# Kernel tuning notes

Measured on AMD Instinct MI355X. Metric: run time of the kernel, lower is better.

## Reference

```python
import jax, jax.numpy as jnp
import numpy as np

N_NODES = 50000
N_EDGES = 1600000
IN_DIM = 128
N_HEADS = 8
OUT_DIM = 16


def setup_inputs() -> dict:
    key = jax.random.key(0)
    ks = jax.random.split(key, 9)
    scale = 1.0 / np.sqrt(IN_DIM)
    return {
        "state": jax.random.normal(ks[0], (N_NODES, IN_DIM), dtype=jnp.float32),
        "src": jax.random.randint(ks[1], (N_EDGES,), 0, N_NODES, dtype=jnp.int32),
        "dst": jax.random.randint(ks[2], (N_EDGES,), 0, N_NODES, dtype=jnp.int32),
        "WQ": jax.random.normal(ks[3], (IN_DIM, N_HEADS * OUT_DIM), dtype=jnp.float32) * scale,
        "bQ": jnp.zeros((N_HEADS * OUT_DIM,), dtype=jnp.float32),
        "WK": jax.random.normal(ks[4], (IN_DIM, N_HEADS * OUT_DIM), dtype=jnp.float32) * scale,
        "bK": jnp.zeros((N_HEADS * OUT_DIM,), dtype=jnp.float32),
        "WV": jax.random.normal(ks[5], (IN_DIM, N_HEADS * OUT_DIM), dtype=jnp.float32) * scale,
        "bV": jnp.zeros((N_HEADS * OUT_DIM,), dtype=jnp.float32),
    }


def reference(state, src, dst, WQ, bQ, WK, bK, WV, bV):
    N = state.shape[0]
    # node projections -> [N, H, D]
    Qh = (state @ WQ + bQ).reshape(N, N_HEADS, OUT_DIM)
    Kh = (state @ WK + bK).reshape(N, N_HEADS, OUT_DIM)
    Vh = (state @ WV + bV).reshape(N, N_HEADS, OUT_DIM)
    # edge-wise K[src] . Q[dst] per head -> [E, H]
    score = jnp.einsum("ehd,ehd->eh", Kh[src], Qh[dst])
    # scaled, clamped exp (unnormalized attention)
    score = jnp.exp(jnp.clip(score / np.sqrt(OUT_DIM), -5.0, 5.0))  # [E, H]
    # scatter-sum aggregation to destination nodes
    wV = jax.ops.segment_sum(Vh[src] * score[:, :, None], dst, num_segments=N)  # [N, H, D]
    z = jax.ops.segment_sum(score, dst, num_segments=N)  # [N, H]
    return wV / z[:, :, None]
```

## Files before the change

### kernel.cpp

```cpp
#include <hip/hip_runtime.h>

#define NNODES 50000
#define NEDGES 1600000
#define NB 196
#define BCAP 10240

typedef __attribute__((ext_vector_type(8))) short short8;
typedef __attribute__((ext_vector_type(4))) float fp32x4;

#if defined(__has_builtin)
#if __has_builtin(__builtin_amdgcn_sdot4)
#define HAVE_SDOT4 1
#endif
#endif

__device__ __forceinline__ unsigned short f2bf(float f) {
    unsigned int u = __float_as_uint(f);
    u += 0x7fffu + ((u >> 16) & 1u);
    return (unsigned short)(u >> 16);
}

__device__ __forceinline__ float sb2f(unsigned int u, int j) {
    return (float)((int)(u << (24 - 8 * j)) >> 24);
}

__global__ __launch_bounds__(128) void cast_wt(
    const float* __restrict__ WQ, const float* __restrict__ WK,
    const float* __restrict__ WV, unsigned short* __restrict__ WT,
    int* __restrict__ gcur)
{
    if (blockIdx.x == 0) {
        gcur[threadIdx.x] = 0;
        gcur[threadIdx.x + 128] = 0;
    }
    const int w = blockIdx.x >> 7;
    const int n = blockIdx.x & 127;
    const int k = threadIdx.x;
    const float* W = (w == 0) ? WQ : ((w == 1) ? WK : WV);
    WT[w * 16384 + n * 128 + k] = f2bf(W[k * 128 + n]);
}

__global__ __launch_bounds__(256) void proj_mfma(
    const float* __restrict__ state, const unsigned short* __restrict__ WT,
    const float* __restrict__ bQ, const float* __restrict__ bK,
    const float* __restrict__ bV,
    unsigned char* __restrict__ Qbi, unsigned char* __restrict__ KVb,
    float* __restrict__ scl)
{
    __shared__ float smem[4 * 16 * 132];
    unsigned short* lwt = (unsigned short*)smem;
    float* lbuf = smem;

    const int tid  = threadIdx.x;
    const int wv   = tid >> 6;
    const int lane = tid & 63;
    const int lm   = lane & 15;
    const int quad = lane >> 4;
    const int m0   = blockIdx.x * 64 + wv * 16;
    const int m    = m0 + lm;

    fp32x4 acc[3][8];
#pragma unroll
    for (int w = 0; w < 3; ++w)
#pragma unroll
        for (int t = 0; t < 8; ++t)
            acc[w][t] = (fp32x4){0.f, 0.f, 0.f, 0.f};

    const int kq = quad * 8;
#pragma unroll
    for (int kb = 0; kb < 128; kb += 32) {
        uint4 bstg[6];
#pragma unroll
        for (int j = 0; j < 6; ++j) {
            const int s = tid + 256 * j;
            const int slm = s & 15, squad = (s >> 4) & 3, stw = s >> 6;
            bstg[j] = *(const uint4*)(WT + (stw >> 3) * 16384
                                         + ((stw & 7) * 16 + slm) * 128
                                         + kb + squad * 8);
        }
        short8 a = (short8){0,0,0,0,0,0,0,0};
        if (m < NNODES) {
            const float4 f0 = *(const float4*)(state + (size_t)m * 128 + kb + kq);
            const float4 f1 = *(const float4*)(state + (size_t)m * 128 + kb + kq + 4);
            a[0] = (short)f2bf(f0.x); a[1] = (short)f2bf(f0.y);
            a[2] = (short)f2bf(f0.z); a[3] = (short)f2bf(f0.w);
            a[4] = (short)f2bf(f1.x); a[5] = (short)f2bf(f1.y);
            a[6] = (short)f2bf(f1.z); a[7] = (short)f2bf(f1.w);
        }
#pragma unroll
        for (int j = 0; j < 6; ++j)
            *(uint4*)((char*)lwt + (tid + 256 * j) * 16) = bstg[j];
        __syncthreads();
#pragma unroll
        for (int w = 0; w < 3; ++w) {
#pragma unroll
            for (int t = 0; t < 8; ++t) {
                const short8 b = *(const short8*)((char*)lwt + ((w * 8 + t) * 64 + lane) * 16);
                acc[w][t] = __builtin_amdgcn_mfma_f32_16x16x32_bf16(a, b, acc[w][t], 0, 0, 0);
            }
        }
        __syncthreads();
    }

    const int rrow = lane >> 2;
    const int rcol = (lane & 3) * 32;
    const int grow = m0 + rrow;
#pragma unroll
    for (int w = 0; w < 3; ++w) {
        const float* bp = (w == 0) ? bQ : ((w == 1) ? bK : bV);
        float* L = lbuf + wv * (16 * 132);
#pragma unroll
        for (int t = 0; t < 8; ++t) {
            const float bb = bp[t * 16 + lm];
#pragma unroll
            for (int r = 0; r < 4; ++r)
                L[(quad * 4 + r) * 132 + t * 16 + lm] = acc[w][t][r] + bb;
        }
        __syncthreads();
        if (grow < NNODES) {
            float xv[32];
#pragma unroll
            for (int c = 0; c < 4; ++c) {
                const float* lp = &L[rrow * 132 + rcol + c * 8];
                const float4 x0 = *(const float4*)(lp);
                const float4 x1 = *(const float4*)(lp + 4);
                xv[c*8+0] = x0.x; xv[c*8+1] = x0.y; xv[c*8+2] = x0.z; xv[c*8+3] = x0.w;
                xv[c*8+4] = x1.x; xv[c*8+5] = x1.y; xv[c*8+6] = x1.z; xv[c*8+7] = x1.w;
            }
            float mx = 0.f;
#pragma unroll
            for (int j = 0; j < 32; ++j) mx = fmaxf(mx, fabsf(xv[j]));
            mx = fmaxf(mx, __shfl_xor(mx, 1));
            mx = fmaxf(mx, __shfl_xor(mx, 2));
            const float inv = (mx > 0.f) ? 127.0f / mx : 0.f;
            unsigned int du[8];
#pragma unroll
            for (int d = 0; d < 8; ++d) {
                const int b0 = (int)rintf(xv[d*4 + 0] * inv);
                const int b1 = (int)rintf(xv[d*4 + 1] * inv);
                const int b2 = (int)rintf(xv[d*4 + 2] * inv);
                const int b3 = (int)rintf(xv[d*4 + 3] * inv);
                du[d] = (unsigned)(b0 & 255) | ((unsigned)(b1 & 255) << 8)
                      | ((unsigned)(b2 & 255) << 16) | ((unsigned)(b3 & 255) << 24);
            }
            unsigned char* gp;
            if (w == 0)      gp = Qbi + (size_t)grow * 128 + rcol;
            else if (w == 1) gp = KVb + (size_t)grow * 256 + rcol;
            else             gp = KVb + (size_t)grow * 256 + 128 + rcol;
            *(uint4*)(gp)      = (uint4){du[0], du[1], du[2], du[3]};
            *(uint4*)(gp + 16) = (uint4){du[4], du[5], du[6], du[7]};
            if ((lane & 3) == 0) {
                if (w == 0)      scl[(size_t)grow * 4 + 2] = mx * (1.0f / 127.0f);
                else if (w == 1) scl[(size_t)grow * 4 + 0] = mx * (1.0f / 508.0f);
                else             scl[(size_t)grow * 4 + 1] = mx * (1.0f / 127.0f);
            }
        }
        __syncthreads();
    }
}

__global__ __launch_bounds__(256) void bucket_pass1(
    const int* __restrict__ src, const int* __restrict__ dst,
    int* __restrict__ gcur, int* __restrict__ pbuf)
{
    __shared__ int hist[256];
    __shared__ int lofs[256];
    __shared__ int gbase[256];
    __shared__ int wsum[4];
    __shared__ int pktg[2048];

    const int t = threadIdx.x;
    hist[t] = 0;
    __syncthreads();

    const long long e0 = (long long)blockIdx.x * 2048 + t * 8;
    const bool valid = (e0 < NEDGES);
    unsigned int w8[8]; int b8[8], r8[8];
    if (valid) {
        const int4 sA = *(const int4*)(src + e0);
        const int4 sB = *(const int4*)(src + e0 + 4);
        const int4 dA = *(const int4*)(dst + e0);
        const int4 dB = *(const int4*)(dst + e0 + 4);
        const int dd[8] = {dA.x, dA.y, dA.z, dA.w, dB.x, dB.y, dB.z, dB.w};
        const int ss[8] = {sA.x, sA.y, sA.z, sA.w, sB.x, sB.y, sB.z, sB.w};
#pragma unroll
        for (int j = 0; j < 8; ++j) {
            const int bb = dd[j] >> 8;
            b8[j] = bb;
            w8[j] = ((unsigned)bb << 24) | ((unsigned)ss[j] << 8) | (unsigned)(dd[j] & 255);
            r8[j] = atomicAdd(&hist[bb], 1);
        }
    }
    __syncthreads();

    const int v = hist[t];
    if (t < NB && v > 0) gbase[t] = atomicAdd(&gcur[t], v);

    int x = v;
#pragma unroll
    for (int off = 1; off < 64; off <<= 1) {
        const int y = __shfl_up(x, off);
        if ((t & 63) >= off) x += y;
    }
    if ((t & 63) == 63) wsum[t >> 6] = x;
    __syncthreads();
    int pre = 0;
#pragma unroll
    for (int ww = 0; ww < 4; ++ww)
        if (ww < (t >> 6)) pre += wsum[ww];
    const int tot = wsum[0] + wsum[1] + wsum[2] + wsum[3];
    lofs[t] = x + pre - v;
    __syncthreads();

    if (valid) {
#pragma unroll
        for (int j = 0; j < 8; ++j)
            pktg[lofs[b8[j]] + r8[j]] = (int)w8[j];
    }
    __syncthreads();

#pragma unroll
    for (int j = 0; j < 8; ++j) {
        const int slot = t + 256 * j;
        if (slot < tot) {
            const unsigned int w = (unsigned int)pktg[slot];
            const int bb = (int)(w >> 24);
            const long long g = (long long)bb * BCAP + gbase[bb] + (slot - lofs[bb]);
            pbuf[g] = (int)(w & 0x00FFFFFFu);
        }
    }
}

__global__ __launch_bounds__(1024) void bucket_pass2(
    const int* __restrict__ pbuf, const int* __restrict__ gcur,
    int* __restrict__ eidx, int2* __restrict__ offs2)
{
    __shared__ int hist[256];
    __shared__ int cur[256];
    __shared__ int wsum[4];
    __shared__ int pstash[BCAP];

    const int b = blockIdx.x;
    const int t = threadIdx.x;
    int cnt = gcur[b];
    if (cnt > BCAP) cnt = BCAP;
    const long long base = (long long)b * BCAP;

    if (t < 256) hist[t] = 0;
    __syncthreads();

    for (int i = t; i < cnt; i += 1024) {
        const int g = pbuf[base + i];
        pstash[i] = g;
        atomicAdd(&hist[g & 255], 1);
    }
    __syncthreads();

    int x = 0, v = 0;
    if (t < 256) {
        v = hist[t];
        x = v;
#pragma unroll
        for (int off = 1; off < 64; off <<= 1) {
            const int y = __shfl_up(x, off);
            if ((t & 63) >= off) x += y;
        }
        if ((t & 63) == 63) wsum[t >> 6] = x;
    }
    __syncthreads();
    if (t < 256) {
        int pre = 0;
#pragma unroll
        for (int ww = 0; ww < 4; ++ww)
            if (ww < (t >> 6)) pre += wsum[ww];
        const int ex = x + pre - v;
        cur[t] = ex;
        const int n = b * 256 + t;
        if (n < NNODES) {
            int2 oe; oe.x = (int)(base + ex); oe.y = (int)(base + ex + v);
            offs2[n] = oe;
        }
    }
    __syncthreads();

    for (int i = t; i < cnt; i += 1024) {
        const int g = pstash[i];
        const int p = atomicAdd(&cur[g & 255], 1);
        eidx[base + p] = g >> 8;
    }
}

__global__ __launch_bounds__(256) void aggregate_kernel(
    const int* __restrict__ eidx, const int2* __restrict__ offs2,
    const unsigned char* __restrict__ Qbi, const unsigned char* __restrict__ KVb,
    const float* __restrict__ scl, float* __restrict__ out)
{
    const int n = blockIdx.x * 4 + (threadIdx.x >> 6);
    const int l = threadIdx.x & 63;
    if (n >= NNODES) return;
    const int eo = l >> 3;
    const int h  = l & 7;

    const uint4 qw = *(const uint4*)(Qbi + (size_t)n * 128 + h * 16);
    const float qf = scl[(size_t)n * 4 + 2];
#ifndef HAVE_SDOT4
    float q[16];
    q[0]  = sb2f(qw.x, 0); q[1]  = sb2f(qw.x, 1); q[2]  = sb2f(qw.x, 2); q[3]  = sb2f(qw.x, 3);
    q[4]  = sb2f(qw.y, 0); q[5]  = sb2f(qw.y, 1); q[6]  = sb2f(qw.y, 2); q[7]  = sb2f(qw.y, 3);
    q[8]  = sb2f(qw.z, 0); q[9]  = sb2f(qw.z, 1); q[10] = sb2f(qw.z, 2); q[11] = sb2f(qw.z, 3);
    q[12] = sb2f(qw.w, 0); q[13] = sb2f(qw.w, 1); q[14] = sb2f(qw.w, 2); q[15] = sb2f(qw.w, 3);
#endif

    const int2 oe = offs2[n];
    const int beg = oe.x, end = oe.y;

    float acc[16];
#pragma unroll
    for (int j = 0; j < 16; ++j) acc[j] = 0.f;
    float zacc = 0.f;

    for (int i = beg; i < end; i += 16) {
        const int ei0 = i + eo;
        const int ei1 = ei0 + 8;
        const bool act0 = (ei0 < end);
        const bool act1 = (ei1 < end);
        const int s0 = eidx[act0 ? ei0 : beg];
        const int s1 = eidx[act1 ? ei1 : beg];

        const unsigned char* rp0 = KVb + (size_t)s0 * 256;
        const unsigned char* rp1 = KVb + (size_t)s1 * 256;
        const uint4 kw0 = *(const uint4*)(rp0 + h * 16);
        const uint4 vw0 = *(const uint4*)(rp0 + 128 + h * 16);
        const uint4 kw1 = *(const uint4*)(rp1 + h * 16);
        const uint4 vw1 = *(const uint4*)(rp1 + 128 + h * 16);
        const float2 sc0 = *(const float2*)(scl + (size_t)s0 * 4);
        const float2 sc1 = *(const float2*)(scl + (size_t)s1 * 4);

        float p0, p1;
#ifdef HAVE_SDOT4
        int id0 = __builtin_amdgcn_sdot4((int)kw0.x, (int)qw.x, 0,   false);
        id0     = __builtin_amdgcn_sdot4((int)kw0.y, (int)qw.y, id0, false);
        id0     = __builtin_amdgcn_sdot4((int)kw0.z, (int)qw.z, id0, false);
        id0     = __builtin_amdgcn_sdot4((int)kw0.w, (int)qw.w, id0, false);
        p0 = (float)id0 * (sc0.x * qf);
        int id1 = __builtin_amdgcn_sdot4((int)kw1.x, (int)qw.x, 0,   false);
        id1     = __builtin_amdgcn_sdot4((int)kw1.y, (int)qw.y, id1, false);
        id1     = __builtin_amdgcn_sdot4((int)kw1.z, (int)qw.z, id1, false);
        id1     = __builtin_amdgcn_sdot4((int)kw1.w, (int)qw.w, id1, false);
        p1 = (float)id1 * (sc1.x * qf);
#else
        p0 = sb2f(kw0.x, 0) * q[0];
        p0 = fmaf(sb2f(kw0.x, 1), q[1],  p0); p0 = fmaf(sb2f(kw0.x, 2), q[2],  p0);
        p0 = fmaf(sb2f(kw0.x, 3), q[3],  p0); p0 = fmaf(sb2f(kw0.y, 0), q[4],  p0);
        p0 = fmaf(sb2f(kw0.y, 1), q[5],  p0); p0 = fmaf(sb2f(kw0.y, 2), q[6],  p0);
        p0 = fmaf(sb2f(kw0.y, 3), q[7],  p0); p0 = fmaf(sb2f(kw0.z, 0), q[8],  p0);
        p0 = fmaf(sb2f(kw0.z, 1), q[9],  p0); p0 = fmaf(sb2f(kw0.z, 2), q[10], p0);
        p0 = fmaf(sb2f(kw0.z, 3), q[11], p0); p0 = fmaf(sb2f(kw0.w, 0), q[12], p0);
        p0 = fmaf(sb2f(kw0.w, 1), q[13], p0); p0 = fmaf(sb2f(kw0.w, 2), q[14], p0);
        p0 = fmaf(sb2f(kw0.w, 3), q[15], p0);
        p0 *= sc0.x * qf;
        p1 = sb2f(kw1.x, 0) * q[0];
        p1 = fmaf(sb2f(kw1.x, 1), q[1],  p1); p1 = fmaf(sb2f(kw1.x, 2), q[2],  p1);
        p1 = fmaf(sb2f(kw1.x, 3), q[3],  p1); p1 = fmaf(sb2f(kw1.y, 0), q[4],  p1);
        p1 = fmaf(sb2f(kw1.y, 1), q[5],  p1); p1 = fmaf(sb2f(kw1.y, 2), q[6],  p1);
        p1 = fmaf(sb2f(kw1.y, 3), q[7],  p1); p1 = fmaf(sb2f(kw1.z, 0), q[8],  p1);
        p1 = fmaf(sb2f(kw1.z, 1), q[9],  p1); p1 = fmaf(sb2f(kw1.z, 2), q[10], p1);
        p1 = fmaf(sb2f(kw1.z, 3), q[11], p1); p1 = fmaf(sb2f(kw1.w, 0), q[12], p1);
        p1 = fmaf(sb2f(kw1.w, 1), q[13], p1); p1 = fmaf(sb2f(kw1.w, 2), q[14], p1);
        p1 = fmaf(sb2f(kw1.w, 3), q[15], p1);
        p1 *= sc1.x * qf;
#endif

        float w0 = __expf(fminf(fmaxf(p0, -5.f), 5.f));
        float w1 = __expf(fminf(fmaxf(p1, -5.f), 5.f));
        w0 = act0 ? w0 : 0.f;
        w1 = act1 ? w1 : 0.f;
        zacc += w0 + w1;
        const float wv0 = w0 * sc0.y;
        const float wv1 = w1 * sc1.y;

        acc[0]  = fmaf(sb2f(vw0.x, 0), wv0, acc[0]);  acc[1]  = fmaf(sb2f(vw0.x, 1), wv0, acc[1]);
        acc[2]  = fmaf(sb2f(vw0.x, 2), wv0, acc[2]);  acc[3]  = fmaf(sb2f(vw0.x, 3), wv0, acc[3]);
        acc[4]  = fmaf(sb2f(vw0.y, 0), wv0, acc[4]);  acc[5]  = fmaf(sb2f(vw0.y, 1), wv0, acc[5]);
        acc[6]  = fmaf(sb2f(vw0.y, 2), wv0, acc[6]);  acc[7]  = fmaf(sb2f(vw0.y, 3), wv0, acc[7]);
        acc[8]  = fmaf(sb2f(vw0.z, 0), wv0, acc[8]);  acc[9]  = fmaf(sb2f(vw0.z, 1), wv0, acc[9]);
        acc[10] = fmaf(sb2f(vw0.z, 2), wv0, acc[10]); acc[11] = fmaf(sb2f(vw0.z, 3), wv0, acc[11]);
        acc[12] = fmaf(sb2f(vw0.w, 0), wv0, acc[12]); acc[13] = fmaf(sb2f(vw0.w, 1), wv0, acc[13]);
        acc[14] = fmaf(sb2f(vw0.w, 2), wv0, acc[14]); acc[15] = fmaf(sb2f(vw0.w, 3), wv0, acc[15]);

        acc[0]  = fmaf(sb2f(vw1.x, 0), wv1, acc[0]);  acc[1]  = fmaf(sb2f(vw1.x, 1), wv1, acc[1]);
        acc[2]  = fmaf(sb2f(vw1.x, 2), wv1, acc[2]);  acc[3]  = fmaf(sb2f(vw1.x, 3), wv1, acc[3]);
        acc[4]  = fmaf(sb2f(vw1.y, 0), wv1, acc[4]);  acc[5]  = fmaf(sb2f(vw1.y, 1), wv1, acc[5]);
        acc[6]  = fmaf(sb2f(vw1.y, 2), wv1, acc[6]);  acc[7]  = fmaf(sb2f(vw1.y, 3), wv1, acc[7]);
        acc[8]  = fmaf(sb2f(vw1.z, 0), wv1, acc[8]);  acc[9]  = fmaf(sb2f(vw1.z, 1), wv1, acc[9]);
        acc[10] = fmaf(sb2f(vw1.z, 2), wv1, acc[10]); acc[11] = fmaf(sb2f(vw1.z, 3), wv1, acc[11]);
        acc[12] = fmaf(sb2f(vw1.w, 0), wv1, acc[12]); acc[13] = fmaf(sb2f(vw1.w, 1), wv1, acc[13]);
        acc[14] = fmaf(sb2f(vw1.w, 2), wv1, acc[14]); acc[15] = fmaf(sb2f(vw1.w, 3), wv1, acc[15]);
    }

#pragma unroll
    for (int st = 8; st < 64; st <<= 1) {
        zacc += __shfl_xor(zacc, st);
#pragma unroll
        for (int j = 0; j < 16; ++j) acc[j] += __shfl_xor(acc[j], st);
    }

    if (eo == 0) {
        const float inv = 1.0f / zacc;
        float* op = out + (size_t)n * 128 + h * 16;
        *(float4*)(op)      = make_float4(acc[0]*inv,  acc[1]*inv,  acc[2]*inv,  acc[3]*inv);
        *(float4*)(op + 4)  = make_float4(acc[4]*inv,  acc[5]*inv,  acc[6]*inv,  acc[7]*inv);
        *(float4*)(op + 8)  = make_float4(acc[8]*inv,  acc[9]*inv,  acc[10]*inv, acc[11]*inv);
        *(float4*)(op + 12) = make_float4(acc[12]*inv, acc[13]*inv, acc[14]*inv, acc[15]*inv);
    }
}

extern "C" void kernel_launch(void* const* d_in, const int* in_sizes, int n_in,
                              void* d_out, int out_size, void* d_ws, size_t ws_size,
                              hipStream_t stream)
{
    const float* state = (const float*)d_in[0];
    const int*   src   = (const int*)d_in[1];
    const int*   dst   = (const int*)d_in[2];
    const float* WQ    = (const float*)d_in[3];
    const float* bQ    = (const float*)d_in[4];
    const float* WK    = (const float*)d_in[5];
    const float* bK    = (const float*)d_in[6];
    const float* WV    = (const float*)d_in[7];
    const float* bV    = (const float*)d_in[8];
    float* out = (float*)d_out;

    unsigned char*  Qbi = (unsigned char*)d_ws;
    unsigned char*  KVb = Qbi + (size_t)NNODES * 128;
    float*          scl = (float*)(KVb + (size_t)NNODES * 256);
    unsigned short* WT  = (unsigned short*)(scl + (size_t)NNODES * 4);
    int* pbuf  = (int*)(WT + 3 * 16384);
    int* eidx  = pbuf + (size_t)NB * BCAP;
    int* gcur  = eidx + (size_t)NB * BCAP;
    int2* offs2 = (int2*)(gcur + 256);

    cast_wt<<<3 * 128, 128, 0, stream>>>(WQ, WK, WV, WT, gcur);
    proj_mfma<<<(NNODES + 63) / 64, 256, 0, stream>>>(state, WT, bQ, bK, bV, Qbi, KVb, scl);

    bucket_pass1<<<(NEDGES + 2047) / 2048, 256, 0, stream>>>(src, dst, gcur, pbuf);
    bucket_pass2<<<NB, 1024, 0, stream>>>(pbuf, gcur, eidx, offs2);

    aggregate_kernel<<<(NNODES + 3) / 4, 256, 0, stream>>>(eidx, offs2, Qbi, KVb, scl, out);
}
```

Before: 213.7 us.

## Fuse weight cast with edge bucketing pass and prefetch edge indices in aggregate

Merges the weight transpose/cast kernel and the first bucketing pass into one launch, using block-index ranges to split the work, and zeroes the bucket counters with hipMemsetAsync instead. This removes one kernel launch and lets the small cast work overlap with the edge histogramming. The aggregate loop now software-prefetches the next iteration's source indices, so the eidx load latency is hidden behind the current gather. The cost is one extra memset call and a few more live registers in the aggregate loop.

```diff
diff --git a/kernel.cpp b/kernel.cpp
--- a/kernel.cpp
+++ b/kernel.cpp
@@ -4,6 +4,8 @@
 #define NEDGES 1600000
 #define NB 196
 #define BCAP 10240
+#define CWB 192
+#define P1B 782
 
 typedef __attribute__((ext_vector_type(8))) short short8;
 typedef __attribute__((ext_vector_type(4))) float fp32x4;
@@ -24,20 +26,90 @@
     return (float)((int)(u << (24 - 8 * j)) >> 24);
 }
 
-__global__ __launch_bounds__(128) void cast_wt(
+__global__ __launch_bounds__(256) void wt_p1(
     const float* __restrict__ WQ, const float* __restrict__ WK,
     const float* __restrict__ WV, unsigned short* __restrict__ WT,
-    int* __restrict__ gcur)
+    const int* __restrict__ src, const int* __restrict__ dst,
+    int* __restrict__ gcur, int* __restrict__ pbuf)
 {
-    if (blockIdx.x == 0) {
-        gcur[threadIdx.x] = 0;
-        gcur[threadIdx.x + 128] = 0;
-    }
-    const int w = blockIdx.x >> 7;
-    const int n = blockIdx.x & 127;
-    const int k = threadIdx.x;
-    const float* W = (w == 0) ? WQ : ((w == 1) ? WK : WV);
-    WT[w * 16384 + n * 128 + k] = f2bf(W[k * 128 + n]);
+    __shared__ int hist[256];
+    __shared__ int lofs[256];
+    __shared__ int gbase[256];
+    __shared__ int wsum[4];
+    __shared__ int pktg[2048];
+
+    const int t = threadIdx.x;
+
+    if (blockIdx.x < CWB) {
+        const int task = blockIdx.x * 2 + (t >> 7);
+        const int w = task >> 7;
+        const int n = task & 127;
+        const int k = t & 127;
+        const float* W = (w == 0) ? WQ : ((w == 1) ? WK : WV);
+        WT[w * 16384 + n * 128 + k] = f2bf(W[k * 128 + n]);
+        return;
+    }
+    const int bid = blockIdx.x - CWB;
+
+    hist[t] = 0;
+    __syncthreads();
+
+    const long long e0 = (long long)bid * 2048 + t * 8;
+    const bool valid = (e0 < NEDGES);
+    unsigned int w8[8]; int b8[8], r8[8];
+    if (valid) {
+        const int4 sA = *(const int4*)(src + e0);
+        const int4 sB = *(const int4*)(src + e0 + 4);
+        const int4 dA = *(const int4*)(dst + e0);
+        const int4 dB = *(const int4*)(dst + e0 + 4);
+        const int dd[8] = {dA.x, dA.y, dA.z, dA.w, dB.x, dB.y, dB.z, dB.w};
+        const int ss[8] = {sA.x, sA.y, sA.z, sA.w, sB.x, sB.y, sB.z, sB.w};
+#pragma unroll
+        for (int j = 0; j < 8; ++j) {
+            const int bb = dd[j] >> 8;
+            b8[j] = bb;
+            w8[j] = ((unsigned)bb << 24) | ((unsigned)ss[j] << 8) | (unsigned)(dd[j] & 255);
+            r8[j] = atomicAdd(&hist[bb], 1);
+        }
+    }
+    __syncthreads();
+
+    const int v = hist[t];
+    if (t < NB && v > 0) gbase[t] = atomicAdd(&gcur[t], v);
+
+    int x = v;
+#pragma unroll
+    for (int off = 1; off < 64; off <<= 1) {
+        const int y = __shfl_up(x, off);
+        if ((t & 63) >= off) x += y;
+    }
+    if ((t & 63) == 63) wsum[t >> 6] = x;
+    __syncthreads();
+    int pre = 0;
+#pragma unroll
+    for (int ww = 0; ww < 4; ++ww)
+        if (ww < (t >> 6)) pre += wsum[ww];
+    const int tot = wsum[0] + wsum[1] + wsum[2] + wsum[3];
+    lofs[t] = x + pre - v;
+    __syncthreads();
+
+    if (valid) {
+#pragma unroll
+        for (int j = 0; j < 8; ++j)
+            pktg[lofs[b8[j]] + r8[j]] = (int)w8[j];
+    }
+    __syncthreads();
+
+#pragma unroll
+    for (int j = 0; j < 8; ++j) {
+        const int slot = t + 256 * j;
+        if (slot < tot) {
+            const unsigned int w = (unsigned int)pktg[slot];
+            const int bb = (int)(w >> 24);
+            const long long g = (long long)bb * BCAP + gbase[bb] + (slot - lofs[bb]);
+            pbuf[g] = (int)(w & 0x00FFFFFFu);
+        }
+    }
 }
 
 __global__ __launch_bounds__(256) void proj_mfma(
@@ -159,78 +231,6 @@
     }
 }
 
-__global__ __launch_bounds__(256) void bucket_pass1(
-    const int* __restrict__ src, const int* __restrict__ dst,
-    int* __restrict__ gcur, int* __restrict__ pbuf)
-{
-    __shared__ int hist[256];
-    __shared__ int lofs[256];
-    __shared__ int gbase[256];
-    __shared__ int wsum[4];
-    __shared__ int pktg[2048];
-
-    const int t = threadIdx.x;
-    hist[t] = 0;
-    __syncthreads();
-
-    const long long e0 = (long long)blockIdx.x * 2048 + t * 8;
-    const bool valid = (e0 < NEDGES);
-    unsigned int w8[8]; int b8[8], r8[8];
-    if (valid) {
-        const int4 sA = *(const int4*)(src + e0);
-        const int4 sB = *(const int4*)(src + e0 + 4);
-        const int4 dA = *(const int4*)(dst + e0);
-        const int4 dB = *(const int4*)(dst + e0 + 4);
-        const int dd[8] = {dA.x, dA.y, dA.z, dA.w, dB.x, dB.y, dB.z, dB.w};
-        const int ss[8] = {sA.x, sA.y, sA.z, sA.w, sB.x, sB.y, sB.z, sB.w};
-#pragma unroll
-        for (int j = 0; j < 8; ++j) {
-            const int bb = dd[j] >> 8;
-            b8[j] = bb;
-            w8[j] = ((unsigned)bb << 24) | ((unsigned)ss[j] << 8) | (unsigned)(dd[j] & 255);
-            r8[j] = atomicAdd(&hist[bb], 1);
-        }
-    }
-    __syncthreads();
-
-    const int v = hist[t];
-    if (t < NB && v > 0) gbase[t] = atomicAdd(&gcur[t], v);
-
-    int x = v;
-#pragma unroll
-    for (int off = 1; off < 64; off <<= 1) {
-        const int y = __shfl_up(x, off);
-        if ((t & 63) >= off) x += y;
-    }
-    if ((t & 63) == 63) wsum[t >> 6] = x;
-    __syncthreads();
-    int pre = 0;
-#pragma unroll
-    for (int ww = 0; ww < 4; ++ww)
-        if (ww < (t >> 6)) pre += wsum[ww];
-    const int tot = wsum[0] + wsum[1] + wsum[2] + wsum[3];
-    lofs[t] = x + pre - v;
-    __syncthreads();
-
-    if (valid) {
-#pragma unroll
-        for (int j = 0; j < 8; ++j)
-            pktg[lofs[b8[j]] + r8[j]] = (int)w8[j];
-    }
-    __syncthreads();
-
-#pragma unroll
-    for (int j = 0; j < 8; ++j) {
-        const int slot = t + 256 * j;
-        if (slot < tot) {
-            const unsigned int w = (unsigned int)pktg[slot];
-            const int bb = (int)(w >> 24);
-            const long long g = (long long)bb * BCAP + gbase[bb] + (slot - lofs[bb]);
-            pbuf[g] = (int)(w & 0x00FFFFFFu);
-        }
-    }
-}
-
 __global__ __launch_bounds__(1024) void bucket_pass2(
     const int* __restrict__ pbuf, const int* __restrict__ gcur,
     int* __restrict__ eidx, int2* __restrict__ offs2)
@@ -301,6 +301,14 @@
     const int eo = l >> 3;
     const int h  = l & 7;
 
+    const int2 oe = offs2[n];
+    const int beg = oe.x, end = oe.y;
+
+    const int pi0 = beg + eo;
+    const int pi1 = pi0 + 8;
+    int s0 = eidx[(pi0 < end) ? pi0 : beg];
+    int s1 = eidx[(pi1 < end) ? pi1 : beg];
+
     const uint4 qw = *(const uint4*)(Qbi + (size_t)n * 128 + h * 16);
     const float qf = scl[(size_t)n * 4 + 2];
 #ifndef HAVE_SDOT4
@@ -311,30 +319,30 @@
     q[12] = sb2f(qw.w, 0); q[13] = sb2f(qw.w, 1); q[14] = sb2f(qw.w, 2); q[15] = sb2f(qw.w, 3);
 #endif
 
-    const int2 oe = offs2[n];
-    const int beg = oe.x, end = oe.y;
-
     float acc[16];
 #pragma unroll
     for (int j = 0; j < 16; ++j) acc[j] = 0.f;
     float zacc = 0.f;
 
     for (int i = beg; i < end; i += 16) {
-        const int ei0 = i + eo;
-        const int ei1 = ei0 + 8;
-        const bool act0 = (ei0 < end);
-        const bool act1 = (ei1 < end);
-        const int s0 = eidx[act0 ? ei0 : beg];
-        const int s1 = eidx[act1 ? ei1 : beg];
-
-        const unsigned char* rp0 = KVb + (size_t)s0 * 256;
-        const unsigned char* rp1 = KVb + (size_t)s1 * 256;
+        const bool act0 = (i + eo < end);
+        const bool act1 = (i + eo + 8 < end);
+        const int cs0 = s0;
+        const int cs1 = s1;
+
+        const int ni0 = i + 16 + eo;
+        const int ni1 = ni0 + 8;
+        s0 = eidx[(ni0 < end) ? ni0 : beg];
+        s1 = eidx[(ni1 < end) ? ni1 : beg];
+
+        const unsigned char* rp0 = KVb + (size_t)cs0 * 256;
+        const unsigned char* rp1 = KVb + (size_t)cs1 * 256;
         const uint4 kw0 = *(const uint4*)(rp0 + h * 16);
         const uint4 vw0 = *(const uint4*)(rp0 + 128 + h * 16);
         const uint4 kw1 = *(const uint4*)(rp1 + h * 16);
         const uint4 vw1 = *(const uint4*)(rp1 + 128 + h * 16);
-        const float2 sc0 = *(const float2*)(scl + (size_t)s0 * 4);
-        const float2 sc1 = *(const float2*)(scl + (size_t)s1 * 4);
+        const float2 sc0 = *(const float2*)(scl + (size_t)cs0 * 4);
+        const float2 sc1 = *(const float2*)(scl + (size_t)cs1 * 4);
 
         float p0, p1;
 #ifdef HAVE_SDOT4
@@ -439,11 +447,9 @@
     int* gcur  = eidx + (size_t)NB * BCAP;
     int2* offs2 = (int2*)(gcur + 256);
 
-    cast_wt<<<3 * 128, 128, 0, stream>>>(WQ, WK, WV, WT, gcur);
+    hipMemsetAsync(gcur, 0, 256 * sizeof(int), stream);
+    wt_p1<<<CWB + P1B, 256, 0, stream>>>(WQ, WK, WV, WT, src, dst, gcur, pbuf);
     proj_mfma<<<(NNODES + 63) / 64, 256, 0, stream>>>(state, WT, bQ, bK, bV, Qbi, KVb, scl);
-
-    bucket_pass1<<<(NEDGES + 2047) / 2048, 256, 0, stream>>>(src, dst, gcur, pbuf);
     bucket_pass2<<<NB, 1024, 0, stream>>>(pbuf, gcur, eidx, offs2);
-
     aggregate_kernel<<<(NNODES + 3) / 4, 256, 0, stream>>>(eidx, offs2, Qbi, KVb, scl, out);
 }
```

Result: no change. 210.7 us (-1.4%).
